# Performance work log

Measured on AMD Instinct MI355X. Metric: run time of the kernel, lower is better.

## Reference

```python
import jax, jax.numpy as jnp
import numpy as np

B, TQ, TB, C, H, INNER = 4, 4096, 2048, 512, 8, 2048
D = C // H


def _ln(x, g, b, eps=1e-5):
    m = x.mean(-1, keepdims=True)
    v = ((x - m) ** 2).mean(-1, keepdims=True)
    return (x - m) / jnp.sqrt(v + eps) * g + b


def _heads(t):
    b, t_, _ = t.shape
    return t.reshape(b, t_, H, D).transpose(0, 2, 1, 3)  # (B,h,T,d)


def _merge(t):
    b, _, t_, _ = t.shape
    return t.transpose(0, 2, 1, 3).reshape(b, t_, C)


def _lin(x, w, b):
    return x @ w + b


def _forward(x, y0, y1,
             ln1_g, ln1_b, ln2_0_g, ln2_0_b, ln2_1_g, ln2_1_b,
             ln3_g, ln3_b, ln4_g, ln4_b, ln5_g, ln5_b,
             ca_q_w, ca_q_b, ca_k0_w, ca_k0_b, ca_v0_w, ca_v0_b,
             ca_k1_w, ca_k1_b, ca_v1_w, ca_v1_b, ca_p_w, ca_p_b,
             sa_q_w, sa_q_b, sa_k_w, sa_k_b, sa_v_w, sa_v_b, sa_p_w, sa_p_b,
             m1_w1, m1_b1, m1_w2, m1_b2, m2_w1, m2_b1, m2_w2, m2_b2):
    # ---- cross-attention (LinearCrossAttention, accumulate over branches) ----
    xn = _ln(x, ln1_g, ln1_b)
    q = jax.nn.softmax(_heads(_lin(xn, ca_q_w, ca_q_b)), axis=-1)  # (B,h,TQ,d)
    out = q
    branches = [(y0, ln2_0_g, ln2_0_b, ca_k0_w, ca_k0_b, ca_v0_w, ca_v0_b),
                (y1, ln2_1_g, ln2_1_b, ca_k1_w, ca_k1_b, ca_v1_w, ca_v1_b)]
    for yi, g, bb, kw, kb, vw, vb in branches:
        yn = _ln(yi, g, bb)
        k = jax.nn.softmax(_heads(_lin(yn, kw, kb)), axis=-1)  # (B,h,TB,d)
        v = _heads(_lin(yn, vw, vb))
        k_sum = k.sum(axis=-2, keepdims=True)                   # (B,h,1,d)
        d_inv = 1.0 / jnp.clip((q * k_sum).sum(-1, keepdims=True), 1e-9)
        ctx = jnp.einsum('bhtd,bhte->bhde', k, v)               # (B,h,d,d)
        out = out + (q @ ctx) * d_inv
    x = x + _lin(_merge(out), ca_p_w, ca_p_b)

    # ---- MLP 1 ----
    h1 = _lin(_ln(x, ln3_g, ln3_b), m1_w1, m1_b1)
    x = x + _lin(jax.nn.gelu(h1, approximate=False), m1_w2, m1_b2)

    # ---- self-attention (LinearAttention, attn_type='l1') ----
    xn = _ln(x, ln4_g, ln4_b)
    q = jax.nn.softmax(_heads(_lin(xn, sa_q_w, sa_q_b)), axis=-1)
    k = jax.nn.softmax(_heads(_lin(xn, sa_k_w, sa_k_b)), axis=-1)
    v = _heads(_lin(xn, sa_v_w, sa_v_b))
    k_sum = k.sum(axis=-2, keepdims=True)
    d_inv = 1.0 / (q * k_sum).sum(-1, keepdims=True)
    ctx = jnp.einsum('bhtd,bhte->bhde', k, v)
    sa = (q @ ctx) * d_inv + q
    x = x + _lin(_merge(sa), sa_p_w, sa_p_b)

    # ---- MLP 2 ----
    h2 = _lin(_ln(x, ln5_g, ln5_b), m2_w1, m2_b1)
    x = x + _lin(jax.nn.gelu(h2, approximate=False), m2_w2, m2_b2)
    return x


def setup_inputs() -> dict:
    key = jax.random.key(0)
    ks = iter(jax.random.split(key, 64))
    s = 1.0 / np.sqrt(C)
    si = 1.0 / np.sqrt(INNER)

    def lin_p(din, dout, scale):
        return (jax.random.normal(next(ks), (din, dout), jnp.float32) * scale,
                jnp.zeros((dout,), jnp.float32))

    inp = {
        'x': jax.random.normal(next(ks), (B, TQ, C), jnp.float32),
        'y0': jax.random.normal(next(ks), (B, TB, C), jnp.float32),
        'y1': jax.random.normal(next(ks), (B, TB, C), jnp.float32),
    }
    for nm in ['ln1', 'ln2_0', 'ln2_1', 'ln3', 'ln4', 'ln5']:
        inp[nm + '_g'] = jnp.ones((C,), jnp.float32)
        inp[nm + '_b'] = jnp.zeros((C,), jnp.float32)
    for nm in ['ca_q', 'ca_k0', 'ca_v0', 'ca_k1', 'ca_v1', 'ca_p',
               'sa_q', 'sa_k', 'sa_v', 'sa_p']:
        w, b = lin_p(C, C, s)
        inp[nm + '_w'] = w
        inp[nm + '_b'] = b
    for nm in ['m1', 'm2']:
        w1, b1 = lin_p(C, INNER, s)
        w2, b2 = lin_p(INNER, C, si)
        inp[nm + '_w1'], inp[nm + '_b1'] = w1, b1
        inp[nm + '_w2'], inp[nm + '_b2'] = w2, b2
    return inp


def reference(x, y0, y1,
              ln1_g, ln1_b, ln2_0_g, ln2_0_b, ln2_1_g, ln2_1_b,
              ln3_g, ln3_b, ln4_g, ln4_b, ln5_g, ln5_b,
              ca_q_w, ca_q_b, ca_k0_w, ca_k0_b, ca_v0_w, ca_v0_b,
              ca_k1_w, ca_k1_b, ca_v1_w, ca_v1_b, ca_p_w, ca_p_b,
              sa_q_w, sa_q_b, sa_k_w, sa_k_b, sa_v_w, sa_v_b, sa_p_w, sa_p_b,
              m1_w1, m1_b1, m1_w2, m1_b2, m2_w1, m2_b1, m2_w2, m2_b2):
    return _forward(x, y0, y1,
                    ln1_g, ln1_b, ln2_0_g, ln2_0_b, ln2_1_g, ln2_1_b,
                    ln3_g, ln3_b, ln4_g, ln4_b, ln5_g, ln5_b,
                    ca_q_w, ca_q_b, ca_k0_w, ca_k0_b, ca_v0_w, ca_v0_b,
                    ca_k1_w, ca_k1_b, ca_v1_w, ca_v1_b, ca_p_w, ca_p_b,
                    sa_q_w, sa_q_b, sa_k_w, sa_k_b, sa_v_w, sa_v_b, sa_p_w, sa_p_b,
                    m1_w1, m1_b1, m1_w2, m1_b2, m2_w1, m2_b1, m2_w2, m2_b2)
```

## Files before the change

### kernel.cpp

```cpp
#include <hip/hip_runtime.h>
#include <hip/hip_bf16.h>
#include <math.h>

#define NBATCH 4
#define TQD 4096
#define TBD 2048
#define CDIM 512
#define NH 8
#define HD 64
#define NINNER 2048

using short8 = __attribute__((ext_vector_type(8))) short;
using f32x4  = __attribute__((ext_vector_type(4))) float;

__device__ __forceinline__ float b2f(short s) {
  return __uint_as_float(((unsigned)(unsigned short)s) << 16);
}
__device__ __forceinline__ short f2b(float f) {
  unsigned u = __float_as_uint(f);
  return (short)((u + 0x7FFFu + ((u >> 16) & 1u)) >> 16);
}
__device__ __forceinline__ unsigned pk2(float a, float b) {
  float2 t; t.x = a; t.y = b;
  __hip_bfloat162 h = __float22bfloat162_rn(t);
  return *(unsigned*)&h;
}
__device__ __forceinline__ float gelu_fast(float x) {
  float x3 = x * x * x;
  float y2 = 1.5957691216f * (x + 0.044715f * x3);
  float e = __expf(y2);
  return x * e / (e + 1.0f);
}
__device__ __forceinline__ void gload16(const short* g, short* l) {
  __builtin_amdgcn_global_load_lds((const __attribute__((address_space(1))) void*)g,
                                   (__attribute__((address_space(3))) void*)l, 16, 0, 0);
}

__launch_bounds__(256)
__global__ void ln_kernel(const float* __restrict__ x, const float* __restrict__ g,
                          const float* __restrict__ b, short* __restrict__ out)
{
  int row = blockIdx.x * 4 + (threadIdx.x >> 6);
  int lane = threadIdx.x & 63;
  const float4* xp = (const float4*)(x + (size_t)row * CDIM);
  float4 v0 = xp[lane], v1 = xp[lane + 64];
  float s  = v0.x + v0.y + v0.z + v0.w + v1.x + v1.y + v1.z + v1.w;
  float s2 = v0.x * v0.x + v0.y * v0.y + v0.z * v0.z + v0.w * v0.w
           + v1.x * v1.x + v1.y * v1.y + v1.z * v1.z + v1.w * v1.w;
#pragma unroll
  for (int m = 1; m < 64; m <<= 1) { s += __shfl_xor(s, m); s2 += __shfl_xor(s2, m); }
  float mean = s * (1.0f / CDIM);
  float var  = s2 * (1.0f / CDIM) - mean * mean;
  float inv  = rsqrtf(var + 1e-5f);
  float4 g0 = ((const float4*)g)[lane], g1 = ((const float4*)g)[lane + 64];
  float4 b0 = ((const float4*)b)[lane], b1 = ((const float4*)b)[lane + 64];
  uint2 o0, o1;
  o0.x = pk2((v0.x - mean) * inv * g0.x + b0.x, (v0.y - mean) * inv * g0.y + b0.y);
  o0.y = pk2((v0.z - mean) * inv * g0.z + b0.z, (v0.w - mean) * inv * g0.w + b0.w);
  o1.x = pk2((v1.x - mean) * inv * g1.x + b1.x, (v1.y - mean) * inv * g1.y + b1.y);
  o1.y = pk2((v1.z - mean) * inv * g1.z + b1.z, (v1.w - mean) * inv * g1.w + b1.w);
  uint2* op = (uint2*)(out + (size_t)row * CDIM);
  op[lane] = o0;
  op[lane + 64] = o1;
}

struct TcvtDesc {
  const float* src[14];
  short* dst[14];
  int K[14], N[14], nblk[14];
};
__launch_bounds__(256)
__global__ void tcvt_all(TcvtDesc d)
{
  int blk = blockIdx.x, wi = 0;
  while (blk >= d.nblk[wi]) { blk -= d.nblk[wi]; wi++; }
  const float* __restrict__ W = d.src[wi];
  short* __restrict__ Wt = d.dst[wi];
  int K = d.K[wi], N = d.N[wi];
  __shared__ float t[32][33];
  int nbk = K >> 5;
  int bk = blk % nbk, bn = blk / nbk;
  int cx = threadIdx.x & 31, cy = threadIdx.x >> 5;
#pragma unroll
  for (int i = 0; i < 4; i++)
    t[cy + 8 * i][cx] = W[(size_t)(bk * 32 + cy + 8 * i) * N + bn * 32 + cx];
  __syncthreads();
#pragma unroll
  for (int i = 0; i < 4; i++)
    Wt[(size_t)(bn * 32 + cy + 8 * i) * K + bk * 32 + cx] = f2b(t[cx][cy + 8 * i]);
}

#define VMW(n) asm volatile("s_waitcnt vmcnt(" #n ")" ::: "memory");

template<int EPI, int NF, int KK>
__launch_bounds__(512, 4)
__global__ void gemm128(const short* __restrict__ A, const short* __restrict__ Bt,
                        const float* __restrict__ bias, const float* __restrict__ resid,
                        void* __restrict__ outp, int M, int N, int smLimit,
                        float* __restrict__ ksumP, int csBase, int Trows)
{
  constexpr int BUFB = NF * 2048;
  constexpr int NT = KK >> 5;
  __shared__ short As[4 * 4096];
  __shared__ short Bs[3 * BUFB];
  int tid = threadIdx.x, lane = tid & 63, wave = tid >> 6;
  int l15 = lane & 15, g = lane >> 4;
  int wr = wave >> 2, wn = wave & 3;
  int nbn = N / (NF * 64);
  int per = gridDim.x >> 3;
  int wg = (blockIdx.x & 7) * per + (blockIdx.x >> 3);
  int bm = wg / nbn, bn = wg % nbn;
  f32x4 acc[4][NF] = {};

  int srcslot = ((lane & 3) ^ ((lane >> 3) & 3)) * 8;
  const short* gA0 = A  + (size_t)(bm * 128 + wave * 16 + (lane >> 2)) * KK + srcslot;
  const short* gB0 = Bt + (size_t)(bn * (NF * 64) + wave * 16 + (lane >> 2)) * KK + srcslot;
  const short* gB1 = gB0 + (size_t)128 * KK;
  short* lA = As + wave * 512;
  short* lB = Bs + wave * 512;

  int rsw = (g ^ ((l15 >> 1) & 3)) * 8;
  const short* raB = As + (wr * 64 + l15) * 32 + rsw;
  const short* rbB = Bs + (wn * (NF * 16) + l15) * 32 + rsw;

  short8 af[2], bfr[NF];

#define STGA1(T) gload16(gA0 + (size_t)(T) * 32, lA + ((T) & 3) * 4096);
#define STGB1(T, BI) { \
    gload16(gB0 + (size_t)(T) * 32, lB + (BI) * BUFB); \
    if constexpr (NF == 4) gload16(gB1 + (size_t)(T) * 32, lB + (BI) * BUFB + 4096); }
#define RDB1(BI) { \
    const short* bp = rbB + (BI) * BUFB; \
    _Pragma("unroll") for (int n = 0; n < NF; n++) \
      bfr[n] = *(const short8*)(bp + n * 512); }
#define RDA1(T, q) { \
    const short* ap = raB + ((T) & 3) * 4096 + (q) * 1024; \
    af[0] = *(const short8*)(ap); af[1] = *(const short8*)(ap + 512); }
#define MFMAQ1(q) { \
    __builtin_amdgcn_s_setprio(1); \
    _Pragma("unroll") for (int n = 0; n < NF; n++) { \
      acc[2*(q)][n]   = __builtin_amdgcn_mfma_f32_16x16x32_bf16(bfr[n], af[0], acc[2*(q)][n], 0, 0, 0); \
      acc[2*(q)+1][n] = __builtin_amdgcn_mfma_f32_16x16x32_bf16(bfr[n], af[1], acc[2*(q)+1][n], 0, 0, 0); } \
    __builtin_amdgcn_s_setprio(0); }
#define VMW_S { if constexpr (NF == 4) { VMW(3) } else { VMW(2) } }
#define BARX1 { __builtin_amdgcn_s_barrier(); __builtin_amdgcn_sched_barrier(0x0E); }
#define BAR21 { __builtin_amdgcn_s_barrier(); }

  STGA1(0); STGB1(0, 0);
  STGA1(1); STGB1(1, 1);
  VMW_S;
  BAR21;

  int bR = 0, bS = 2;
#pragma unroll 4
  for (int t = 0; t < NT - 2; ++t) {
    RDB1(bR); RDA1(t, 0); STGA1(t + 2); STGB1(t + 2, bS); BARX1; MFMAQ1(0); BAR21;
    RDA1(t, 1); VMW_S;                                    BARX1; MFMAQ1(1); BAR21;
    bR = (bR == 2) ? 0 : bR + 1;
    bS = (bS == 2) ? 0 : bS + 1;
  }
  {
    constexpr int B2 = (NT - 2) % 3;
    RDB1(B2); RDA1(NT - 2, 0); BARX1; MFMAQ1(0); BAR21;
    RDA1(NT - 2, 1); VMW(0);   BARX1; MFMAQ1(1); BAR21;
  }
  {
    constexpr int B1 = (NT - 1) % 3;
    RDB1(B1); RDA1(NT - 1, 0); BARX1; MFMAQ1(0); BAR21;
    RDA1(NT - 1, 1);           BARX1; MFMAQ1(1);
  }
#undef STGA1
#undef STGB1
#undef RDB1
#undef RDA1
#undef MFMAQ1
#undef VMW_S
#undef BARX1
#undef BAR21

  int row0 = bm * 128 + wr * 64, col0 = bn * (NF * 64) + wn * (NF * 16);
#pragma unroll
  for (int n = 0; n < NF; n++) {
    f32x4 bz = *(const f32x4*)(bias + col0 + n * 16 + g * 4);
#pragma unroll
    for (int m = 0; m < 4; m++)
#pragma unroll
      for (int r = 0; r < 4; r++) acc[m][n][r] += bz[r];
  }
  if (EPI == 0) {
    bool insm = (bn * (NF * 64) < smLimit);
    if constexpr (NF == 4) {
      if (insm) {
#pragma unroll
        for (int m = 0; m < 4; m++) {
          float mx = acc[m][0][0];
#pragma unroll
          for (int n = 0; n < 4; n++)
#pragma unroll
            for (int r = 0; r < 4; r++) mx = fmaxf(mx, acc[m][n][r]);
          mx = fmaxf(mx, __shfl_xor(mx, 16));
          mx = fmaxf(mx, __shfl_xor(mx, 32));
          float s = 0.0f;
#pragma unroll
          for (int n = 0; n < 4; n++)
#pragma unroll
            for (int r = 0; r < 4; r++) {
              float e = __expf(acc[m][n][r] - mx);
              acc[m][n][r] = e; s += e;
            }
          s += __shfl_xor(s, 16);
          s += __shfl_xor(s, 32);
          float inv = 1.0f / s;
#pragma unroll
          for (int n = 0; n < 4; n++)
#pragma unroll
            for (int r = 0; r < 4; r++) acc[m][n][r] *= inv;
        }
      }
    } else {
      if (insm) {
        float* xch = (float*)As;
        float pm[4], ps[4];
#pragma unroll
        for (int m = 0; m < 4; m++) {
          float mx = acc[m][0][0];
#pragma unroll
          for (int n = 0; n < 2; n++)
#pragma unroll
            for (int r = 0; r < 4; r++) mx = fmaxf(mx, acc[m][n][r]);
          mx = fmaxf(mx, __shfl_xor(mx, 16));
          mx = fmaxf(mx, __shfl_xor(mx, 32));
          pm[m] = mx;
        }
        __syncthreads();
        if (g == 0)
#pragma unroll
          for (int m = 0; m < 4; m++) xch[wave * 64 + m * 16 + l15] = pm[m];
        __syncthreads();
#pragma unroll
        for (int m = 0; m < 4; m++)
          pm[m] = fmaxf(pm[m], xch[(wave ^ 1) * 64 + m * 16 + l15]);
#pragma unroll
        for (int m = 0; m < 4; m++) {
          float s = 0.0f;
#pragma unroll
          for (int n = 0; n < 2; n++)
#pragma unroll
            for (int r = 0; r < 4; r++) {
              float e = __expf(acc[m][n][r] - pm[m]);
              acc[m][n][r] = e; s += e;
            }
          s += __shfl_xor(s, 16);
          s += __shfl_xor(s, 32);
          ps[m] = s;
        }
        __syncthreads();
        if (g == 0)
#pragma unroll
          for (int m = 0; m < 4; m++) xch[wave * 64 + m * 16 + l15] = ps[m];
        __syncthreads();
#pragma unroll
        for (int m = 0; m < 4; m++) {
          float inv = 1.0f / (ps[m] + xch[(wave ^ 1) * 64 + m * 16 + l15]);
#pragma unroll
          for (int n = 0; n < 2; n++)
#pragma unroll
            for (int r = 0; r < 4; r++) acc[m][n][r] *= inv;
        }
      }
    }
  }
  if (EPI == 0 && ksumP != nullptr) {
    unsigned rel = (unsigned)(col0 - csBase);
    if (rel < 512u) {
      float* kp = ksumP + ((row0 / Trows) * 8 + (int)(rel >> 6)) * 64 + (int)(rel & 63u);
#pragma unroll
      for (int n = 0; n < NF; n++) {
        f32x4 s = acc[0][n];
#pragma unroll
        for (int m = 1; m < 4; m++)
#pragma unroll
          for (int r = 0; r < 4; r++) s[r] += acc[m][n][r];
#pragma unroll
        for (int msk = 1; msk < 16; msk <<= 1)
#pragma unroll
          for (int r = 0; r < 4; r++) s[r] += __shfl_xor(s[r], msk);
        if (l15 == 0)
#pragma unroll
          for (int r = 0; r < 4; r++)
            atomicAdd(kp + n * 16 + g * 4 + r, s[r]);
      }
    }
  }
  if (EPI == 1) {
#pragma unroll
    for (int m = 0; m < 4; m++)
#pragma unroll
      for (int n = 0; n < NF; n++)
#pragma unroll
        for (int r = 0; r < 4; r++) acc[m][n][r] = gelu_fast(acc[m][n][r]);
  }
#pragma unroll
  for (int m = 0; m < 4; m++) {
    int row = row0 + m * 16 + l15;
#pragma unroll
    for (int n = 0; n < NF; n++) {
      size_t base = (size_t)row * N + col0 + n * 16 + g * 4;
      if (EPI == 2) {
        f32x4 rv = *(const f32x4*)(resid + base);
        f32x4 o;
#pragma unroll
        for (int r = 0; r < 4; r++) o[r] = rv[r] + acc[m][n][r];
        *(f32x4*)((float*)outp + base) = o;
      } else {
        uint2 u;
        u.x = pk2(acc[m][n][0], acc[m][n][1]);
        u.y = pk2(acc[m][n][2], acc[m][n][3]);
        *(uint2*)((unsigned short*)outp + base) = u;
      }
    }
  }
}

#define LDC 40
__launch_bounds__(256)
__global__ void ctx_kernel(const short* __restrict__ k, const short* __restrict__ v,
                           float* __restrict__ ctx, int T, int parts, int SD)
{
  __shared__ short kT[4][64 * LDC];
  __shared__ short vT[4][64 * LDC];
  int bh = blockIdx.x & 31, part = blockIdx.x >> 5;
  int b = bh >> 3, h = bh & 7;
  int tid = threadIdx.x, lane = tid & 63, wave = tid >> 6;
  int l15 = lane & 15, g = lane >> 4;
  int tlen = T / (4 * parts);
  int tbeg = (part * 4 + wave) * tlen;
  f32x4 acc[4][4] = {};
  short* myK = kT[wave];
  short* myV = vT[wave];
  for (int t0 = tbeg; t0 < tbeg + tlen; t0 += 32) {
#pragma unroll
    for (int j = 0; j < 4; j++) {
      int c = lane + j * 64;
      int r = c >> 3, d0 = (c & 7) * 8;
      short8 kv = *(const short8*)(k + (size_t)(b * T + t0 + r) * SD + h * 64 + d0);
      short8 vv = *(const short8*)(v + (size_t)(b * T + t0 + r) * SD + h * 64 + d0);
#pragma unroll
      for (int i = 0; i < 8; i++) {
        myK[(d0 + i) * LDC + r] = kv[i];
        myV[(d0 + i) * LDC + r] = vv[i];
      }
    }
    __syncthreads();
    short8 af[4], bfr[4];
#pragma unroll
    for (int m = 0; m < 4; m++) af[m]  = *(const short8*)(myK + (m * 16 + l15) * LDC + g * 8);
#pragma unroll
    for (int n = 0; n < 4; n++) bfr[n] = *(const short8*)(myV + (n * 16 + l15) * LDC + g * 8);
#pragma unroll
    for (int m = 0; m < 4; m++)
#pragma unroll
      for (int n = 0; n < 4; n++)
        acc[m][n] = __builtin_amdgcn_mfma_f32_16x16x32_bf16(af[m], bfr[n], acc[m][n], 0, 0, 0);
    __syncthreads();
  }
  float* cp = ctx + (size_t)bh * 64 * 64;
#pragma unroll
  for (int m = 0; m < 4; m++)
#pragma unroll
    for (int n = 0; n < 4; n++)
#pragma unroll
      for (int r = 0; r < 4; r++)
        atomicAdd(cp + (m * 16 + g * 4 + r) * 64 + (n * 16 + l15), acc[m][n][r]);
}

#define LQ 72
__launch_bounds__(256)
__global__ void qctx_kernel(const short* __restrict__ q,
                            const float* __restrict__ ctx,
                            const float* __restrict__ ksum,
                            short* __restrict__ outp, int T, int nb, int SD)
{
  __shared__ short qs[128 * LQ];
  __shared__ short cT[2][64 * LQ];
  __shared__ float dls[2][128];
  int ntb = T >> 7;
  int bh = blockIdx.x / ntb, tq = blockIdx.x % ntb;
  int b = bh >> 3, h = bh & 7;
  int tid = threadIdx.x, lane = tid & 63, wave = tid >> 6;
  int l15 = lane & 15, g = lane >> 4;
  size_t qbase = (size_t)(b * T + tq * 128) * SD + h * 64;
  size_t obase = (size_t)(b * T + tq * 128) * CDIM + h * 64;

#pragma unroll
  for (int j = 0; j < 4; j++) {
    int c = tid + j * 256;
    int r = c >> 3, d0 = (c & 7) * 8;
    *(short8*)(qs + r * LQ + d0) = *(const short8*)(q + qbase + (size_t)r * SD + d0);
  }
  for (int br = 0; br < nb; br++) {
    const float* cp = ctx + ((size_t)br * 32 + bh) * 4096;
#pragma unroll
    for (int j = 0; j < 16; j++) {
      int e2 = tid + j * 256;
      int dd = e2 >> 6, ee = e2 & 63;
      cT[br][ee * LQ + dd] = f2b(cp[e2]);
    }
  }
  __syncthreads();

  int r0 = wave * 32;
  for (int br = 0; br < nb; br++) {
    int row = r0 + (lane >> 1);
    int dbase = (lane & 1) * 32;
    const float* kp = ksum + ((size_t)br * 32 + bh) * 64 + dbase;
    float s = 0.0f;
#pragma unroll
    for (int d = 0; d < 32; d++)
      s += b2f(qs[row * LQ + dbase + d]) * kp[d];
    s += __shfl_xor(s, 1);
    if (!(lane & 1)) dls[br][row] = 1.0f / fmaxf(s, 1e-9f);
  }

  short8 af[2][2];
#pragma unroll
  for (int m = 0; m < 2; m++)
#pragma unroll
    for (int kk = 0; kk < 2; kk++)
      af[m][kk] = *(const short8*)(qs + (r0 + m * 16 + l15) * LQ + kk * 32 + g * 8);

  float ofin[2][4][4];
#pragma unroll
  for (int m = 0; m < 2; m++)
#pragma unroll
    for (int n = 0; n < 4; n++)
#pragma unroll
      for (int r = 0; r < 4; r++)
        ofin[m][n][r] = b2f(qs[(r0 + m * 16 + g * 4 + r) * LQ + n * 16 + l15]);

  for (int br = 0; br < nb; br++) {
    f32x4 acc[2][4] = {};
#pragma unroll
    for (int kk = 0; kk < 2; kk++) {
      short8 bfr[4];
#pragma unroll
      for (int n = 0; n < 4; n++)
        bfr[n] = *(const short8*)(cT[br] + (n * 16 + l15) * LQ + kk * 32 + g * 8);
#pragma unroll
      for (int m = 0; m < 2; m++)
#pragma unroll
        for (int n = 0; n < 4; n++)
          acc[m][n] = __builtin_amdgcn_mfma_f32_16x16x32_bf16(af[m][kk], bfr[n], acc[m][n], 0, 0, 0);
    }
#pragma unroll
    for (int m = 0; m < 2; m++)
#pragma unroll
      for (int n = 0; n < 4; n++)
#pragma unroll
        for (int r = 0; r < 4; r++)
          ofin[m][n][r] += dls[br][r0 + m * 16 + g * 4 + r] * acc[m][n][r];
  }

#pragma unroll
  for (int m = 0; m < 2; m++)
#pragma unroll
    for (int n = 0; n < 4; n++)
#pragma unroll
      for (int r = 0; r < 4; r++) {
        int row = r0 + m * 16 + g * 4 + r;
        int col = n * 16 + l15;
        outp[obase + (size_t)row * CDIM + col] = f2b(ofin[m][n][r]);
      }
}

extern "C" void kernel_launch(void* const* d_in, const int* in_sizes, int n_in,
                              void* d_out, int out_size, void* d_ws, size_t ws_size,
                              hipStream_t stream)
{
  (void)in_sizes; (void)n_in; (void)out_size; (void)ws_size;
  const float* x     = (const float*)d_in[0];
  const float* y0    = (const float*)d_in[1];
  const float* y1    = (const float*)d_in[2];
  const float* ln1g  = (const float*)d_in[3];
  const float* ln1b  = (const float*)d_in[4];
  const float* ln20g = (const float*)d_in[5];
  const float* ln20b = (const float*)d_in[6];
  const float* ln21g = (const float*)d_in[7];
  const float* ln21b = (const float*)d_in[8];
  const float* ln3g  = (const float*)d_in[9];
  const float* ln3b  = (const float*)d_in[10];
  const float* ln4g  = (const float*)d_in[11];
  const float* ln4b  = (const float*)d_in[12];
  const float* ln5g  = (const float*)d_in[13];
  const float* ln5b  = (const float*)d_in[14];
  const float* caqw  = (const float*)d_in[15];
  const float* caqb  = (const float*)d_in[16];
  const float* cak0w = (const float*)d_in[17];
  const float* cak0b = (const float*)d_in[18];
  const float* cav0w = (const float*)d_in[19];
  const float* cav0b = (const float*)d_in[20];
  const float* cak1w = (const float*)d_in[21];
  const float* cak1b = (const float*)d_in[22];
  const float* cav1w = (const float*)d_in[23];
  const float* cav1b = (const float*)d_in[24];
  const float* capw  = (const float*)d_in[25];
  const float* capb  = (const float*)d_in[26];
  const float* saqw  = (const float*)d_in[27];
  const float* saqb  = (const float*)d_in[28];
  const float* sakw  = (const float*)d_in[29];
  const float* sakb  = (const float*)d_in[30];
  const float* savw  = (const float*)d_in[31];
  const float* savb  = (const float*)d_in[32];
  const float* sapw  = (const float*)d_in[33];
  const float* sapb  = (const float*)d_in[34];
  const float* m1w1  = (const float*)d_in[35];
  const float* m1b1  = (const float*)d_in[36];
  const float* m1w2  = (const float*)d_in[37];
  const float* m1b2  = (const float*)d_in[38];
  const float* m2w1  = (const float*)d_in[39];
  const float* m2b1  = (const float*)d_in[40];
  const float* m2w2  = (const float*)d_in[41];
  const float* m2b2  = (const float*)d_in[42];
  float* xout = (float*)d_out;

  char* p = (char*)d_ws;
  size_t off = 0;
  auto take = [&](size_t bytes) {
    char* r = p + off;
    off += (bytes + 255) & ~(size_t)255;
    return r;
  };
  const size_t W512 = (size_t)512 * 512 * 2;
  const size_t WMLP = (size_t)2048 * 512 * 2;
  short* wt_caq   = (short*)take(W512);
  short* wt_cakv0 = (short*)take(2 * W512);
  short* wt_cakv1 = (short*)take(2 * W512);
  short* wt_cap   = (short*)take(W512);
  short* wt_saqkv = (short*)take(3 * W512);
  short* wt_sap   = (short*)take(W512);
  short* wt_m1w1  = (short*)take(WMLP);
  short* wt_m1w2  = (short*)take(WMLP);
  short* wt_m2w1  = (short*)take(WMLP);
  short* wt_m2w2  = (short*)take(WMLP);
  float* b_saqkv  = (float*)take(1536 * 4);
  float* b_cakv0  = (float*)take(1024 * 4);
  float* b_cakv1  = (float*)take(1024 * 4);
  short* xn   = (short*)take((size_t)16384 * 512 * 2);
  short* bufD = (short*)take((size_t)16384 * 512 * 2);
  short* big  = (short*)take((size_t)16384 * 1536 * 2);
  short* h1   = (short*)take((size_t)16384 * 2048 * 2);
  float* ksum = (float*)take((size_t)2 * 32 * 64 * 4);
  float* ctxb = (float*)take((size_t)2 * 32 * 64 * 64 * 4);

  short* q_ca  = big;
  short* kv_ca = big + (size_t)8 * 1024 * 1024;
  short* qkv   = big;

  const int MQ  = NBATCH * TQD;
  const int MKV = NBATCH * TBD;

  {
    TcvtDesc d;
    const float* srcs[14] = {caqw, cak0w, cav0w, cak1w, cav1w, capw,
                             saqw, sakw, savw, sapw, m1w1, m1w2, m2w1, m2w2};
    short* dsts[14] = {wt_caq, wt_cakv0, wt_cakv0 + 512 * 512,
                       wt_cakv1, wt_cakv1 + 512 * 512, wt_cap,
                       wt_saqkv, wt_saqkv + 512 * 512, wt_saqkv + 2 * 512 * 512, wt_sap,
                       wt_m1w1, wt_m1w2, wt_m2w1, wt_m2w2};
    int Ks[14] = {512,512,512,512,512,512,512,512,512,512, 512,2048,512,2048};
    int Ns[14] = {512,512,512,512,512,512,512,512,512,512, 2048,512,2048,512};
    int total = 0;
    for (int i = 0; i < 14; i++) {
      d.src[i] = srcs[i]; d.dst[i] = dsts[i]; d.K[i] = Ks[i]; d.N[i] = Ns[i];
      d.nblk[i] = (Ks[i] >> 5) * (Ns[i] >> 5);
      total += d.nblk[i];
    }
    tcvt_all<<<total, 256, 0, stream>>>(d);
  }
  hipMemcpyAsync(b_saqkv,        saqb,  512 * 4, hipMemcpyDeviceToDevice, stream);
  hipMemcpyAsync(b_saqkv + 512,  sakb,  512 * 4, hipMemcpyDeviceToDevice, stream);
  hipMemcpyAsync(b_saqkv + 1024, savb,  512 * 4, hipMemcpyDeviceToDevice, stream);
  hipMemcpyAsync(b_cakv0,        cak0b, 512 * 4, hipMemcpyDeviceToDevice, stream);
  hipMemcpyAsync(b_cakv0 + 512,  cav0b, 512 * 4, hipMemcpyDeviceToDevice, stream);
  hipMemcpyAsync(b_cakv1,        cak1b, 512 * 4, hipMemcpyDeviceToDevice, stream);
  hipMemcpyAsync(b_cakv1 + 512,  cav1b, 512 * 4, hipMemcpyDeviceToDevice, stream);

  ln_kernel<<<MQ / 4, 256, 0, stream>>>(x, ln1g, ln1b, xn);
  hipMemsetAsync(ksum, 0, (size_t)2 * 32 * 64 * 4, stream);
  hipMemsetAsync(ctxb, 0, (size_t)2 * 32 * 64 * 64 * 4, stream);
  gemm128<0, 2, 512><<<512, 512, 0, stream>>>(xn, wt_caq, caqb, nullptr, q_ca,
                                              MQ, 512, 512, nullptr, 0, 0);
  for (int br = 0; br < 2; br++) {
    const float* yy = br ? y1 : y0;
    const float* lg = br ? ln21g : ln20g;
    const float* lb = br ? ln21b : ln20b;
    const short* wk = br ? wt_cakv1 : wt_cakv0;
    const float* bk = br ? b_cakv1 : b_cakv0;
    ln_kernel<<<MKV / 4, 256, 0, stream>>>(yy, lg, lb, bufD);
    gemm128<0, 2, 512><<<512, 512, 0, stream>>>(bufD, wk, bk, nullptr, kv_ca,
                                                MKV, 1024, 512,
                                                ksum + (size_t)br * 2048, 0, TBD);
    ctx_kernel<<<256, 256, 0, stream>>>(kv_ca, kv_ca + 512,
                                        ctxb + (size_t)br * 32 * 4096, TBD, 8, 1024);
  }
  qctx_kernel<<<32 * (TQD / 128), 256, 0, stream>>>(q_ca, ctxb, ksum, bufD, TQD, 2, 512);
  gemm128<2, 2, 512><<<512, 512, 0, stream>>>(bufD, wt_cap, capb, x, xout,
                                              MQ, 512, 0, nullptr, 0, 0);

  ln_kernel<<<MQ / 4, 256, 0, stream>>>(xout, ln3g, ln3b, xn);
  gemm128<1, 4, 512><<<1024, 512, 0, stream>>>(xn, wt_m1w1, m1b1, nullptr, h1,
                                               MQ, 2048, 0, nullptr, 0, 0);
  gemm128<2, 2, 2048><<<512, 512, 0, stream>>>(h1, wt_m1w2, m1b2, xout, xout,
                                               MQ, 512, 0, nullptr, 0, 0);

  ln_kernel<<<MQ / 4, 256, 0, stream>>>(xout, ln4g, ln4b, xn);
  hipMemsetAsync(ksum, 0, (size_t)32 * 64 * 4, stream);
  hipMemsetAsync(ctxb, 0, (size_t)32 * 64 * 64 * 4, stream);
  gemm128<0, 4, 512><<<768, 512, 0, stream>>>(xn, wt_saqkv, b_saqkv, nullptr, qkv,
                                              MQ, 1536, 1024, ksum, 512, TQD);
  ctx_kernel<<<256, 256, 0, stream>>>(qkv + 512, qkv + 1024, ctxb, TQD, 8, 1536);
  qctx_kernel<<<32 * (TQD / 128), 256, 0, stream>>>(qkv, ctxb, ksum, bufD, TQD, 1, 1536);
  gemm128<2, 2, 512><<<512, 512, 0, stream>>>(bufD, wt_sap, sapb, xout, xout,
                                              MQ, 512, 0, nullptr, 0, 0);

  ln_kernel<<<MQ / 4, 256, 0, stream>>>(xout, ln5g, ln5b, xn);
  gemm128<1, 4, 512><<<1024, 512, 0, stream>>>(xn, wt_m2w1, m2b1, nullptr, h1,
                                               MQ, 2048, 0, nullptr, 0, 0);
  gemm128<2, 2, 2048><<<512, 512, 0, stream>>>(h1, wt_m2w2, m2b2, xout, xout,
                                               MQ, 512, 0, nullptr, 0, 0);
}
```

Measured before the change: 550.6 us.

## Load GEMM B fragments directly from global into registers, bypassing LDS

The B (weight) operand is no longer staged through a triple-buffered LDS array. Each wave now loads its own MFMA B fragments straight from global memory into double-buffered registers one K-tile ahead, while A keeps its LDS path. The barrier schedule and vmcnt waits are reworked to fit this. This removes LDS traffic and LDS space for B, but waves sharing the same B columns now fetch duplicate data from global or cache, and register pressure rises.

```diff
diff --git a/kernel.cpp b/kernel.cpp
--- a/kernel.cpp
+++ b/kernel.cpp
@@ -99,10 +99,8 @@
                         void* __restrict__ outp, int M, int N, int smLimit,
                         float* __restrict__ ksumP, int csBase, int Trows)
 {
-  constexpr int BUFB = NF * 2048;
   constexpr int NT = KK >> 5;
   __shared__ short As[4 * 4096];
-  __shared__ short Bs[3 * BUFB];
   int tid = threadIdx.x, lane = tid & 63, wave = tid >> 6;
   int l15 = lane & 15, g = lane >> 4;
   int wr = wave >> 2, wn = wave & 3;
@@ -113,70 +111,63 @@
   f32x4 acc[4][NF] = {};
 
   int srcslot = ((lane & 3) ^ ((lane >> 3) & 3)) * 8;
-  const short* gA0 = A  + (size_t)(bm * 128 + wave * 16 + (lane >> 2)) * KK + srcslot;
-  const short* gB0 = Bt + (size_t)(bn * (NF * 64) + wave * 16 + (lane >> 2)) * KK + srcslot;
-  const short* gB1 = gB0 + (size_t)128 * KK;
+  const short* gA0 = A + (size_t)(bm * 128 + wave * 16 + (lane >> 2)) * KK + srcslot;
   short* lA = As + wave * 512;
-  short* lB = Bs + wave * 512;
-
   int rsw = (g ^ ((l15 >> 1) & 3)) * 8;
   const short* raB = As + (wr * 64 + l15) * 32 + rsw;
-  const short* rbB = Bs + (wn * (NF * 16) + l15) * 32 + rsw;
-
-  short8 af[2], bfr[NF];
+
+  const short* gB[NF];
+#pragma unroll
+  for (int n = 0; n < NF; n++)
+    gB[n] = Bt + (size_t)(bn * (NF * 64) + wn * (NF * 16) + n * 16 + l15) * KK + g * 8;
+
+  short8 af[2], bA[NF], bB[NF];
 
 #define STGA1(T) gload16(gA0 + (size_t)(T) * 32, lA + ((T) & 3) * 4096);
-#define STGB1(T, BI) { \
-    gload16(gB0 + (size_t)(T) * 32, lB + (BI) * BUFB); \
-    if constexpr (NF == 4) gload16(gB1 + (size_t)(T) * 32, lB + (BI) * BUFB + 4096); }
-#define RDB1(BI) { \
-    const short* bp = rbB + (BI) * BUFB; \
-    _Pragma("unroll") for (int n = 0; n < NF; n++) \
-      bfr[n] = *(const short8*)(bp + n * 512); }
+#define LDB(T, Y) { _Pragma("unroll") for (int n = 0; n < NF; n++) \
+    Y[n] = *(const short8*)(gB[n] + (size_t)(T) * 32); }
 #define RDA1(T, q) { \
     const short* ap = raB + ((T) & 3) * 4096 + (q) * 1024; \
     af[0] = *(const short8*)(ap); af[1] = *(const short8*)(ap + 512); }
-#define MFMAQ1(q) { \
+#define MFMAQ1(q, X) { \
     __builtin_amdgcn_s_setprio(1); \
     _Pragma("unroll") for (int n = 0; n < NF; n++) { \
-      acc[2*(q)][n]   = __builtin_amdgcn_mfma_f32_16x16x32_bf16(bfr[n], af[0], acc[2*(q)][n], 0, 0, 0); \
-      acc[2*(q)+1][n] = __builtin_amdgcn_mfma_f32_16x16x32_bf16(bfr[n], af[1], acc[2*(q)+1][n], 0, 0, 0); } \
+      acc[2*(q)][n]   = __builtin_amdgcn_mfma_f32_16x16x32_bf16(X[n], af[0], acc[2*(q)][n], 0, 0, 0); \
+      acc[2*(q)+1][n] = __builtin_amdgcn_mfma_f32_16x16x32_bf16(X[n], af[1], acc[2*(q)+1][n], 0, 0, 0); } \
     __builtin_amdgcn_s_setprio(0); }
-#define VMW_S { if constexpr (NF == 4) { VMW(3) } else { VMW(2) } }
+#define VMW_S  { if constexpr (NF == 4) { VMW(5) } else { VMW(3) } }
+#define VMW_P2 { if constexpr (NF == 4) { VMW(4) } else { VMW(2) } }
 #define BARX1 { __builtin_amdgcn_s_barrier(); __builtin_amdgcn_sched_barrier(0x0E); }
-#define BAR21 { __builtin_amdgcn_s_barrier(); }
-
-  STGA1(0); STGB1(0, 0);
-  STGA1(1); STGB1(1, 1);
-  VMW_S;
-  BAR21;
-
-  int bR = 0, bS = 2;
-#pragma unroll 4
-  for (int t = 0; t < NT - 2; ++t) {
-    RDB1(bR); RDA1(t, 0); STGA1(t + 2); STGB1(t + 2, bS); BARX1; MFMAQ1(0); BAR21;
-    RDA1(t, 1); VMW_S;                                    BARX1; MFMAQ1(1); BAR21;
-    bR = (bR == 2) ? 0 : bR + 1;
-    bS = (bS == 2) ? 0 : bS + 1;
-  }
-  {
-    constexpr int B2 = (NT - 2) % 3;
-    RDB1(B2); RDA1(NT - 2, 0); BARX1; MFMAQ1(0); BAR21;
-    RDA1(NT - 2, 1); VMW(0);   BARX1; MFMAQ1(1); BAR21;
-  }
-  {
-    constexpr int B1 = (NT - 1) % 3;
-    RDB1(B1); RDA1(NT - 1, 0); BARX1; MFMAQ1(0); BAR21;
-    RDA1(NT - 1, 1);           BARX1; MFMAQ1(1);
-  }
+#define TILE(T, X, Y) { \
+    RDA1(T, 0); LDB((T) + 1, Y); STGA1((T) + 2); VMW_S; BARX1; \
+    MFMAQ1(0, X); RDA1(T, 1); MFMAQ1(1, X); }
+#define TILE_P2(T, X, Y) { \
+    RDA1(T, 0); LDB((T) + 1, Y); VMW_P2; BARX1; \
+    MFMAQ1(0, X); RDA1(T, 1); MFMAQ1(1, X); }
+#define TILE_LAST(T, X) { \
+    RDA1(T, 0); VMW(0); \
+    MFMAQ1(0, X); RDA1(T, 1); MFMAQ1(1, X); }
+
+  LDB(0, bA); STGA1(0); STGA1(1);
+  VMW(1);
+  __builtin_amdgcn_s_barrier();
+
+  for (int i = 0; i < (NT - 2) / 2; ++i) {
+    TILE(2 * i,     bA, bB);
+    TILE(2 * i + 1, bB, bA);
+  }
+  TILE_P2(NT - 2, bA, bB);
+  TILE_LAST(NT - 1, bB);
 #undef STGA1
-#undef STGB1
-#undef RDB1
+#undef LDB
 #undef RDA1
 #undef MFMAQ1
 #undef VMW_S
+#undef VMW_P2
 #undef BARX1
-#undef BAR21
+#undef TILE
+#undef TILE_P2
+#undef TILE_LAST
 
   int row0 = bm * 128 + wr * 64, col0 = bn * (NF * 64) + wn * (NF * 16);
 #pragma unroll
```

After: 702.4 us. 1.28x slower.
